# Performance work log

Hardware: AMD Instinct MI355X
Metric: run time of the kernel (lower is better)

The kernel has to match this reference:

```python
import jax, jax.numpy as jnp
import numpy as np

N_NODES = 100000
N_EDGES = 1600000
NFEAT, NHID, NOUT = 128, 64, 32


def setup_inputs() -> dict:
    key = jax.random.key(0)
    ks = jax.random.split(key, 8)
    x = jax.random.normal(ks[0], (N_NODES, NFEAT), dtype=jnp.float32)
    adj_vals = jax.random.uniform(ks[1], (N_EDGES,), dtype=jnp.float32)
    W1 = jax.random.normal(ks[2], (NFEAT, NHID), dtype=jnp.float32) * (1.0 / np.sqrt(NFEAT))
    b1 = jnp.zeros((NHID,), dtype=jnp.float32)
    W2 = jax.random.normal(ks[3], (NHID, NOUT), dtype=jnp.float32) * (1.0 / np.sqrt(NHID))
    b2 = jnp.zeros((NOUT,), dtype=jnp.float32)
    edge_src = jax.random.randint(ks[4], (N_EDGES,), 0, N_NODES, dtype=jnp.int32)
    edge_dst = jax.random.randint(ks[5], (N_EDGES,), 0, N_NODES, dtype=jnp.int32)
    return {"x": x, "adj_vals": adj_vals, "W1": W1, "b1": b1, "W2": W2,
            "b2": b2, "edge_src": edge_src, "edge_dst": edge_dst}


def spmm(vals, src, dst, dense, n_nodes):
    # out[i, :] = sum_{e : dst[e]==i} vals[e] * dense[src[e], :]
    gathered = dense[src] * vals[:, None]          # [E, D] gather (memory-bound)
    return jax.ops.segment_sum(gathered, dst, num_segments=n_nodes)


def reference(x, adj_vals, W1, b1, W2, b2, edge_src, edge_dst):
    # GraphConvolution 1: support = x @ W1; out = adj @ support + b1; relu
    h = spmm(adj_vals, edge_src, edge_dst, x @ W1, N_NODES) + b1
    h = jax.nn.relu(h)
    # dropout is identity in eval mode (training=False)
    # GraphConvolution 2
    out = spmm(adj_vals, edge_src, edge_dst, h @ W2, N_NODES) + b2
    return out
```

## Files before the change

kernel.cpp:

```cpp
#include <hip/hip_runtime.h>
#include <hip/hip_fp16.h>

#define N_NODES 100000
#define N_EDGES 1600000
#define NFEAT 128
#define NHID 64
#define NOUT 32

#define NPB 256
#define NB ((N_NODES + NPB - 1) / NPB)
#define CAP 4608
#define CCH 4096
#define NCH ((N_EDGES + CCH - 1) / CCH)
#define G1B ((N_NODES / 16 + 7) / 8)
#define SQB (N_NODES / 4)

typedef _Float16 half8 __attribute__((ext_vector_type(8)));
typedef float floatx4 __attribute__((ext_vector_type(4)));

__device__ __forceinline__ int wave_incl_scan(int v, int lane) {
#pragma unroll
    for (int d = 1; d < 64; d <<= 1) {
        int t = __shfl_up(v, d, 64);
        if (lane >= d) v += t;
    }
    return v;
}
__device__ __forceinline__ int block_excl_scan_512(int tsum, int tid, int* w8) {
    const int lane = tid & 63, wid = tid >> 6;
    int incl = wave_incl_scan(tsum, lane);
    if (lane == 63) w8[wid] = incl;
    __syncthreads();
    int wbase = 0;
#pragma unroll
    for (int i = 0; i < 7; ++i)
        if (wid > i) wbase += w8[i];
    return wbase + incl - tsum;
}

__global__ __launch_bounds__(64) void prep_kernel(const float* __restrict__ W1,
                                                  const float* __restrict__ W2,
                                                  __half* __restrict__ wfrag,
                                                  __half* __restrict__ w2frag,
                                                  int* __restrict__ gcur) {
    const int l = threadIdx.x;
    const int b = blockIdx.x;
    if (b < 16) {
        const int ks = b >> 2, ct = b & 3;
        const int kb = ks * 32 + (l >> 4) * 8;
        const int c  = ct * 16 + (l & 15);
        union { __half2 h2[4]; uint4 u; } pk;
#pragma unroll
        for (int j = 0; j < 4; ++j)
            pk.h2[j] = __floats2half2_rn(W1[(kb + 2 * j) * NHID + c],
                                         W1[(kb + 2 * j + 1) * NHID + c]);
        *(uint4*)&wfrag[((size_t)b * 64 + l) * 8] = pk.u;
    } else if (b < 20) {
        const int bb = b - 16;
        const int ks = bb >> 1, ct = bb & 1;
        const int kb = ks * 32 + (l >> 4) * 8;
        const int c  = ct * 16 + (l & 15);
        union { __half2 h2[4]; uint4 u; } pk;
#pragma unroll
        for (int j = 0; j < 4; ++j)
            pk.h2[j] = __floats2half2_rn(W2[(kb + 2 * j) * NOUT + c],
                                         W2[(kb + 2 * j + 1) * NOUT + c]);
        *(uint4*)&w2frag[((size_t)bb * 64 + l) * 8] = pk.u;
    } else {
        int i = (b - 20) * 64 + l;
        if (i < NB) gcur[i] = i * CAP;
    }
}

__global__ __launch_bounds__(512) void g1cs_kernel(const float* __restrict__ x,
                                                   const __half* __restrict__ wfrag,
                                                   __half* __restrict__ support,
                                                   const float* __restrict__ vals,
                                                   const int* __restrict__ src,
                                                   const int* __restrict__ dst,
                                                   int* __restrict__ gcur,
                                                   uint2* __restrict__ recsC) {
    __shared__ int cnt[NB];
    __shared__ int pos[NB];
    const int tid = threadIdx.x;

    if (blockIdx.x < NCH) {
        const int cbase0 = blockIdx.x * CCH;
        for (int i = tid; i < NB; i += 512) cnt[i] = 0;
        int dstv[CCH / 512];
        __syncthreads();
#pragma unroll
        for (int k = 0; k < CCH / 512; ++k) {
            int e = cbase0 + k * 512 + tid;
            int d = (e < N_EDGES) ? dst[e] : -1;
            dstv[k] = d;
            if (d >= 0) atomicAdd(&cnt[d >> 8], 1);
        }
        __syncthreads();
        for (int b = tid; b < NB; b += 512) {
            int c = cnt[b];
            pos[b] = c ? atomicAdd(&gcur[b], c) : 0;
        }
        __syncthreads();
#pragma unroll
        for (int k = 0; k < CCH / 512; ++k) {
            int e = cbase0 + k * 512 + tid;
            int d = dstv[k];
            if (d >= 0) {
                int b = d >> 8;
                int slot = atomicAdd(&pos[b], 1);
                if (slot < (b + 1) * CAP)
                    recsC[slot] = make_uint2((unsigned)src[e] |
                                             ((unsigned)(d & (NPB - 1)) << 17),
                                             __float_as_uint(vals[e]));
            }
        }
    } else {
        const int lane = tid & 63;
        const int tile = (blockIdx.x - NCH) * 8 + (tid >> 6);
        const int n0 = tile * 16;
        if (n0 >= N_NODES) return;

        half8 a[4][4];
#pragma unroll
        for (int ks = 0; ks < 4; ++ks)
#pragma unroll
            for (int ct = 0; ct < 4; ++ct)
                a[ks][ct] = *(const half8*)&wfrag[((size_t)(ks * 4 + ct) * 64 + lane) * 8];

        floatx4 acc[4];
#pragma unroll
        for (int ct = 0; ct < 4; ++ct) acc[ct] = (floatx4){0.f, 0.f, 0.f, 0.f};

        const int node = n0 + (lane & 15);
        const float* xrow = x + (size_t)node * NFEAT + (lane >> 4) * 8;

#pragma unroll
        for (int ks = 0; ks < 4; ++ks) {
            float4 f0 = *(const float4*)(xrow + ks * 32);
            float4 f1 = *(const float4*)(xrow + ks * 32 + 4);
            union { __half2 h2[4]; half8 v; } bv;
            bv.h2[0] = __floats2half2_rn(f0.x, f0.y);
            bv.h2[1] = __floats2half2_rn(f0.z, f0.w);
            bv.h2[2] = __floats2half2_rn(f1.x, f1.y);
            bv.h2[3] = __floats2half2_rn(f1.z, f1.w);
#pragma unroll
            for (int ct = 0; ct < 4; ++ct)
                acc[ct] = __builtin_amdgcn_mfma_f32_16x16x32_f16(a[ks][ct], bv.v, acc[ct], 0, 0, 0);
        }

#pragma unroll
        for (int ct = 0; ct < 4; ++ct) {
            __half* srow = support + (size_t)(ct >> 1) * N_NODES * 32 +
                           (size_t)node * 32 + (ct & 1) * 16 + (lane >> 4) * 4;
            union { __half2 h2[2]; uint2 u; } pk;
            pk.h2[0] = __floats2half2_rn(acc[ct][0], acc[ct][1]);
            pk.h2[1] = __floats2half2_rn(acc[ct][2], acc[ct][3]);
            *(uint2*)srow = pk.u;
        }
    }
}

__global__ __launch_bounds__(512) void fine_sort_kernel(const int* __restrict__ gcur,
                                                        const uint2* __restrict__ recsC,
                                                        unsigned* __restrict__ recs2,
                                                        int* __restrict__ offs,
                                                        int* __restrict__ ends) {
    __shared__ int cnt[NPB];
    __shared__ int cur[NPB];
    __shared__ int w8[8];
    const int tid = threadIdx.x;
    const int b = blockIdx.x;
    const int s = b * CAP;
    const int e = min(gcur[b], s + CAP);
    if (tid < NPB) cnt[tid] = 0;
    __syncthreads();
    for (int i = s + tid; i < e; i += 512)
        atomicAdd(&cnt[(recsC[i].x >> 17) & (NPB - 1)], 1);
    __syncthreads();
    int v = (tid < NPB) ? cnt[tid] : 0;
    int excl = block_excl_scan_512(v, tid, w8);
    if (tid < NPB) {
        cur[tid] = excl;
        const int node = b * NPB + tid;
        if (node < N_NODES) {
            offs[node] = s + excl;
            ends[node] = s + excl + v;
        }
    }
    __syncthreads();
    for (int i = s + tid; i < e; i += 512) {
        uint2 r = recsC[i];
        int dl = (r.x >> 17) & (NPB - 1);
        unsigned hb = (unsigned)__half_as_ushort(__float2half(__uint_as_float(r.y))) & 0x7FFFu;
        int p = atomicAdd(&cur[dl], 1);
        recs2[s + p] = (r.x & 0x1FFFFu) | (hb << 17);
    }
}

__global__ __launch_bounds__(256) void spmm1_kernel(const int* __restrict__ offs,
                                                    const int* __restrict__ ends,
                                                    const unsigned* __restrict__ recs,
                                                    const __half* __restrict__ support,
                                                    const float* __restrict__ b1,
                                                    __half* __restrict__ h) {
    __shared__ float red[4][16][33];
    const int tid = threadIdx.x;
    const int lane = tid & 63;
    const int wid = tid >> 6;
    const int slice = blockIdx.x / SQB;
    const int nq = blockIdx.x - slice * SQB;
    const int d = nq * 4 + wid;
    const int g = lane >> 2, q4 = lane & 3;
    __half2 hacc[4];
#pragma unroll
    for (int j = 0; j < 4; ++j) hacc[j] = __half2half2(__float2half(0.f));

    const int start = offs[d], end = ends[d];
    const char* dbase = (const char*)(support + (size_t)slice * N_NODES * 32) + (q4 << 4);
    for (int e = start + g; e < end; e += 16) {
        unsigned r = recs[e];
        __half2 hv2 = __half2half2(__ushort_as_half((unsigned short)(r >> 17)));
        union { uint4 u; __half2 h2[4]; } rw;
        rw.u = *(const uint4*)(dbase + ((size_t)(r & 0x1FFFFu) << 6));
#pragma unroll
        for (int j = 0; j < 4; ++j)
            hacc[j] = __hfma2(rw.h2[j], hv2, hacc[j]);
    }
#pragma unroll
    for (int j = 0; j < 4; ++j) {
        float2 f = __half22float2(hacc[j]);
        red[wid][g][q4 * 8 + 2 * j]     = f.x;
        red[wid][g][q4 * 8 + 2 * j + 1] = f.y;
    }
    __builtin_amdgcn_wave_barrier();
    const int c = lane & 31, chunk = lane >> 5;
    float s = 0.f;
#pragma unroll
    for (int t = 0; t < 8; ++t) s += red[wid][chunk * 8 + t][c];
    s += __shfl_xor(s, 32, 64);
    if (chunk == 0) {
        float hv = fmaxf(s + b1[slice * 32 + c], 0.f);
        h[(size_t)slice * N_NODES * 32 + (size_t)d * 32 + c] = __float2half(hv);
    }
}

__global__ __launch_bounds__(256) void gemm2_kernel(const __half* __restrict__ h,
                                                    const __half* __restrict__ w2frag,
                                                    __half* __restrict__ s2) {
    const int lane = threadIdx.x & 63;
    const int tile = blockIdx.x * 4 + (threadIdx.x >> 6);
    const int n0 = tile * 16;
    if (n0 >= N_NODES) return;

    half8 a[2][2];
#pragma unroll
    for (int ks = 0; ks < 2; ++ks)
#pragma unroll
        for (int ct = 0; ct < 2; ++ct)
            a[ks][ct] = *(const half8*)&w2frag[((size_t)(ks * 2 + ct) * 64 + lane) * 8];

    floatx4 acc[2];
#pragma unroll
    for (int ct = 0; ct < 2; ++ct) acc[ct] = (floatx4){0.f, 0.f, 0.f, 0.f};

    const int node = n0 + (lane & 15);
    const __half* h0 = h + (size_t)node * 32 + (lane >> 4) * 8;

#pragma unroll
    for (int ks = 0; ks < 2; ++ks) {
        half8 bv = *(const half8*)(h0 + (size_t)ks * N_NODES * 32);
#pragma unroll
        for (int ct = 0; ct < 2; ++ct)
            acc[ct] = __builtin_amdgcn_mfma_f32_16x16x32_f16(a[ks][ct], bv, acc[ct], 0, 0, 0);
    }

    __half* srow = s2 + (size_t)node * NOUT + (lane >> 4) * 4;
#pragma unroll
    for (int ct = 0; ct < 2; ++ct) {
        union { __half2 h2[2]; uint2 u; } pk;
        pk.h2[0] = __floats2half2_rn(acc[ct][0], acc[ct][1]);
        pk.h2[1] = __floats2half2_rn(acc[ct][2], acc[ct][3]);
        *(uint2*)&srow[ct * 16] = pk.u;
    }
}

__global__ __launch_bounds__(256) void spmm2_kernel(const int* __restrict__ offs,
                                                    const int* __restrict__ ends,
                                                    const unsigned* __restrict__ recs,
                                                    const __half* __restrict__ dense,
                                                    const float* __restrict__ b2,
                                                    float* __restrict__ out) {
    __shared__ float red[4][16][33];
    const int tid = threadIdx.x;
    const int lane = tid & 63;
    const int wid = tid >> 6;
    const int d = blockIdx.x * 4 + wid;
    if (d >= N_NODES) return;
    const int g = lane >> 2, q4 = lane & 3;
    __half2 hacc[4];
#pragma unroll
    for (int j = 0; j < 4; ++j) hacc[j] = __half2half2(__float2half(0.f));

    const int start = offs[d], end = ends[d];
    const char* dbase = (const char*)dense + (q4 << 4);
    for (int e = start + g; e < end; e += 16) {
        unsigned r = recs[e];
        __half2 hv2 = __half2half2(__ushort_as_half((unsigned short)(r >> 17)));
        union { uint4 u; __half2 h2[4]; } rw;
        rw.u = *(const uint4*)(dbase + ((size_t)(r & 0x1FFFFu) << 6));
#pragma unroll
        for (int j = 0; j < 4; ++j)
            hacc[j] = __hfma2(rw.h2[j], hv2, hacc[j]);
    }
#pragma unroll
    for (int j = 0; j < 4; ++j) {
        float2 f = __half22float2(hacc[j]);
        red[wid][g][q4 * 8 + 2 * j]     = f.x;
        red[wid][g][q4 * 8 + 2 * j + 1] = f.y;
    }
    __builtin_amdgcn_wave_barrier();
    const int c = lane & 31, chunk = lane >> 5;
    float s = 0.f;
#pragma unroll
    for (int t = 0; t < 8; ++t) s += red[wid][chunk * 8 + t][c];
    s += __shfl_xor(s, 32, 64);
    if (chunk == 0) out[(size_t)d * NOUT + c] = s + b2[c];
}

extern "C" void kernel_launch(void* const* d_in, const int* in_sizes, int n_in,
                              void* d_out, int out_size, void* d_ws, size_t ws_size,
                              hipStream_t stream) {
    const float* x        = (const float*)d_in[0];
    const float* adj_vals = (const float*)d_in[1];
    const float* W1       = (const float*)d_in[2];
    const float* b1       = (const float*)d_in[3];
    const float* W2       = (const float*)d_in[4];
    const float* b2       = (const float*)d_in[5];
    const int*   esrc     = (const int*)d_in[6];
    const int*   edst     = (const int*)d_in[7];
    float*       out      = (float*)d_out;

    char* W = (char*)d_ws;
    __half*   support = (__half*)W;
    __half*   h       = (__half*)(W + 12800000);
    uint2*    recsC   = (uint2*)(W + 25600000);
    unsigned* recs2   = (unsigned*)(W + 25600000 + (size_t)NB * CAP * 8);
    int*      IW      = (int*)(W + 25600000 + (size_t)NB * CAP * 12);
    int*      offs    = IW;
    int*      ends    = IW + 100032;
    int*      gcur    = IW + 200064;
    __half*   wfrag   = (__half*)(IW + 200064 + 512);
    __half*   w2frag  = wfrag + 8192;
    __half*   s2      = support;

    prep_kernel<<<20 + (NB + 63) / 64, 64, 0, stream>>>(W1, W2, wfrag, w2frag, gcur);

    g1cs_kernel<<<NCH + G1B, 512, 0, stream>>>(x, wfrag, support,
                                               adj_vals, esrc, edst, gcur, recsC);

    fine_sort_kernel<<<NB, 512, 0, stream>>>(gcur, recsC, recs2, offs, ends);

    spmm1_kernel<<<2 * SQB, 256, 0, stream>>>(offs, ends, recs2, support, b1, h);

    gemm2_kernel<<<(N_NODES / 16 + 3) / 4, 256, 0, stream>>>(h, w2frag, s2);

    spmm2_kernel<<<(N_NODES + 3) / 4, 256, 0, stream>>>(offs, ends, recs2,
                                                        s2, b2, out);
}
```

Before: 148.6 us.

## Store support and hidden features row-major, one wave per node in spmm1

```diff
diff --git a/kernel.cpp b/kernel.cpp
--- a/kernel.cpp
+++ b/kernel.cpp
@@ -13,7 +13,6 @@
 #define CCH 4096
 #define NCH ((N_EDGES + CCH - 1) / CCH)
 #define G1B ((N_NODES / 16 + 7) / 8)
-#define SQB (N_NODES / 4)
 
 typedef _Float16 half8 __attribute__((ext_vector_type(8)));
 typedef float floatx4 __attribute__((ext_vector_type(4)));
@@ -149,14 +148,13 @@
                 acc[ct] = __builtin_amdgcn_mfma_f32_16x16x32_f16(a[ks][ct], bv.v, acc[ct], 0, 0, 0);
         }
 
+        __half* srow = support + (size_t)node * NHID + (lane >> 4) * 4;
 #pragma unroll
         for (int ct = 0; ct < 4; ++ct) {
-            __half* srow = support + (size_t)(ct >> 1) * N_NODES * 32 +
-                           (size_t)node * 32 + (ct & 1) * 16 + (lane >> 4) * 4;
             union { __half2 h2[2]; uint2 u; } pk;
             pk.h2[0] = __floats2half2_rn(acc[ct][0], acc[ct][1]);
             pk.h2[1] = __floats2half2_rn(acc[ct][2], acc[ct][3]);
-            *(uint2*)srow = pk.u;
+            *(uint2*)&srow[ct * 16] = pk.u;
         }
     }
 }
@@ -201,28 +199,26 @@
 __global__ __launch_bounds__(256) void spmm1_kernel(const int* __restrict__ offs,
                                                     const int* __restrict__ ends,
                                                     const unsigned* __restrict__ recs,
-                                                    const __half* __restrict__ support,
+                                                    const __half* __restrict__ dense,
                                                     const float* __restrict__ b1,
                                                     __half* __restrict__ h) {
-    __shared__ float red[4][16][33];
+    __shared__ float red[4][8][65];
     const int tid = threadIdx.x;
     const int lane = tid & 63;
     const int wid = tid >> 6;
-    const int slice = blockIdx.x / SQB;
-    const int nq = blockIdx.x - slice * SQB;
-    const int d = nq * 4 + wid;
-    const int g = lane >> 2, q4 = lane & 3;
+    const int d = blockIdx.x * 4 + wid;
+    if (d >= N_NODES) return;
+    const int g = lane >> 3, q = lane & 7;
     __half2 hacc[4];
 #pragma unroll
     for (int j = 0; j < 4; ++j) hacc[j] = __half2half2(__float2half(0.f));
 
     const int start = offs[d], end = ends[d];
-    const char* dbase = (const char*)(support + (size_t)slice * N_NODES * 32) + (q4 << 4);
-    for (int e = start + g; e < end; e += 16) {
+    for (int e = start + g; e < end; e += 8) {
         unsigned r = recs[e];
         __half2 hv2 = __half2half2(__ushort_as_half((unsigned short)(r >> 17)));
         union { uint4 u; __half2 h2[4]; } rw;
-        rw.u = *(const uint4*)(dbase + ((size_t)(r & 0x1FFFFu) << 6));
+        rw.u = *(const uint4*)((const char*)dense + ((size_t)(r & 0x1FFFFu) << 7) + (q << 4));
 #pragma unroll
         for (int j = 0; j < 4; ++j)
             hacc[j] = __hfma2(rw.h2[j], hv2, hacc[j]);
@@ -230,19 +226,15 @@
 #pragma unroll
     for (int j = 0; j < 4; ++j) {
         float2 f = __half22float2(hacc[j]);
-        red[wid][g][q4 * 8 + 2 * j]     = f.x;
-        red[wid][g][q4 * 8 + 2 * j + 1] = f.y;
+        red[wid][g][q * 8 + 2 * j]     = f.x;
+        red[wid][g][q * 8 + 2 * j + 1] = f.y;
     }
     __builtin_amdgcn_wave_barrier();
-    const int c = lane & 31, chunk = lane >> 5;
     float s = 0.f;
 #pragma unroll
-    for (int t = 0; t < 8; ++t) s += red[wid][chunk * 8 + t][c];
-    s += __shfl_xor(s, 32, 64);
-    if (chunk == 0) {
-        float hv = fmaxf(s + b1[slice * 32 + c], 0.f);
-        h[(size_t)slice * N_NODES * 32 + (size_t)d * 32 + c] = __float2half(hv);
-    }
+    for (int gg = 0; gg < 8; ++gg) s += red[wid][gg][lane];
+    float hv = fmaxf(s + b1[lane], 0.f);
+    h[(size_t)d * NHID + lane] = __float2half(hv);
 }
 
 __global__ __launch_bounds__(256) void gemm2_kernel(const __half* __restrict__ h,
@@ -265,11 +257,11 @@
     for (int ct = 0; ct < 2; ++ct) acc[ct] = (floatx4){0.f, 0.f, 0.f, 0.f};
 
     const int node = n0 + (lane & 15);
-    const __half* h0 = h + (size_t)node * 32 + (lane >> 4) * 8;
+    const __half* hrow = h + (size_t)node * NHID + (lane >> 4) * 8;
 
 #pragma unroll
     for (int ks = 0; ks < 2; ++ks) {
-        half8 bv = *(const half8*)(h0 + (size_t)ks * N_NODES * 32);
+        half8 bv = *(const half8*)(hrow + ks * 32);
 #pragma unroll
         for (int ct = 0; ct < 2; ++ct)
             acc[ct] = __builtin_amdgcn_mfma_f32_16x16x32_f16(a[ks][ct], bv, acc[ct], 0, 0, 0);
@@ -361,7 +353,8 @@
 
     fine_sort_kernel<<<NB, 512, 0, stream>>>(gcur, recsC, recs2, offs, ends);
 
-    spmm1_kernel<<<2 * SQB, 256, 0, stream>>>(offs, ends, recs2, support, b1, h);
+    spmm1_kernel<<<(N_NODES + 3) / 4, 256, 0, stream>>>(offs, ends, recs2,
+                                                        support, b1, h);
 
     gemm2_kernel<<<(N_NODES / 16 + 3) / 4, 256, 0, stream>>>(h, w2frag, s2);
 
```

After: 131.6 us. -11.4%, faster.
